# Performance work log

Measured on AMD Instinct MI355X. Metric: run time of the kernel, lower is better.

Reference implementation:

```python
import jax, jax.numpy as jnp
import numpy as np

L = 8192   # query length
N = 8192   # key/value length
DK = 128   # head dim = dmodel // h = 2048 // 16
PAD = 128  # number of trailing padded key positions


def setup_inputs() -> dict:
    key = jax.random.key(0)
    kq, kk, kv = jax.random.split(key, 3)
    Q = jax.random.normal(kq, (L, DK), dtype=jnp.float32)
    K = jax.random.normal(kk, (N, DK), dtype=jnp.float32)
    V = jax.random.normal(kv, (N, DK), dtype=jnp.float32)
    # True = masked. Causal mask (strict upper triangle) for self-attention.
    mask_self_attention = ~jnp.tril(jnp.ones((L, N), dtype=bool))
    # Padding mask: last PAD key positions are padding.
    mask_padding = jnp.zeros((L, N), dtype=bool).at[:, N - PAD:].set(True)
    return {"Q": Q, "K": K, "V": V,
            "mask_self_attention": mask_self_attention,
            "mask_padding": mask_padding}


def reference(Q, K, V, mask_self_attention, mask_padding):
    # SDPA(Q,K,V) = softmax(QK^T / sqrt(dk)) V ; dropout is identity in eval.
    scale = 1.0 / np.sqrt(DK).astype(np.float32)
    scores = (Q @ K.T) * scale                       # [L, N]
    scores = jnp.where(mask_self_attention, -jnp.inf, scores)
    scores = jnp.where(mask_padding, -jnp.inf, scores)
    attn = jax.nn.softmax(scores, axis=-1)           # [L, N]
    return attn @ V                                   # [L, DK]
```

## Files before the change

kernel.cpp:

```cpp
#include <hip/hip_runtime.h>
#include <stdint.h>

typedef __attribute__((ext_vector_type(8))) short short8;
typedef __attribute__((ext_vector_type(4))) short s16x4;
typedef __attribute__((ext_vector_type(4))) float f32x4;

#define D_K 128
#define N_KV 8192
#define NT2 64

__device__ __forceinline__ unsigned short f2bf(float x) {
  unsigned int u = __float_as_uint(x);
  u += 0x7FFFu + ((u >> 16) & 1u);
  return (unsigned short)(u >> 16);
}
__device__ __forceinline__ unsigned int pk2(float lo, float hi) {
  return (unsigned int)f2bf(lo) | ((unsigned int)f2bf(hi) << 16);
}
__device__ __forceinline__ unsigned int cvtpk(float lo, float hi) {
  unsigned int r;
  asm("v_cvt_pk_bf16_f32 %0, %1, %2" : "=v"(r) : "v"(lo), "v"(hi));
  return r;
}
__device__ __forceinline__ float bfval(unsigned int u16) {
  return __uint_as_float(u16 << 16);
}
__device__ __forceinline__ f32x4 mfma16(s16x4 a, s16x4 b, f32x4 c) {
  asm("v_mfma_f32_16x16x16_bf16 %0, %1, %2, %0" : "+v"(c) : "v"(a), "v"(b));
  return c;
}
__device__ __forceinline__ void gload16(const void* g, void* l) {
  __builtin_amdgcn_global_load_lds(
      (const __attribute__((address_space(1))) unsigned int*)g,
      (__attribute__((address_space(3))) unsigned int*)l, 16, 0, 0);
}
__device__ __host__ __forceinline__ int nunits64(int t) {
  int n = 4 * t + 4;
  return n > 252 ? 252 : n;
}

__global__ void prep_kernel(const float* __restrict__ Q,
                            const float* __restrict__ K,
                            const float* __restrict__ V,
                            unsigned short* __restrict__ Qb,
                            unsigned short* __restrict__ Kb,
                            unsigned short* __restrict__ Vtb) {
  __shared__ unsigned short tile[64][65];
  const int b = blockIdx.x;
  const int tid = threadIdx.x;
  if (b < 1024) {
    const float scale = (b < 512) ? 0.12751742941349835f : 1.0f;
    const float* src = (b < 512) ? Q : K;
    unsigned short* dst = (b < 512) ? Qb : Kb;
    const int i = (b & 511) * 256 + tid;
    const float4* s = (const float4*)src;
    float4 a = s[2 * i], c4 = s[2 * i + 1];
    uint4 o;
    o.x = pk2(a.x * scale, a.y * scale);
    o.y = pk2(a.z * scale, a.w * scale);
    o.z = pk2(c4.x * scale, c4.y * scale);
    o.w = pk2(c4.z * scale, c4.w * scale);
    *(uint4*)(dst + (size_t)i * 8) = o;
  } else {
    const int bb = b - 1024;
    const int kv0 = (bb >> 1) << 6, dk0 = (bb & 1) << 6;
    const int r = tid >> 2;
    const int c0 = (tid & 3) << 4;
#pragma unroll
    for (int j = 0; j < 4; ++j) {
      float4 v = *(const float4*)(V + (size_t)(kv0 + r) * D_K + dk0 + c0 + 4 * j);
      tile[r][c0 + 4 * j + 0] = f2bf(v.x);
      tile[r][c0 + 4 * j + 1] = f2bf(v.y);
      tile[r][c0 + 4 * j + 2] = f2bf(v.z);
      tile[r][c0 + 4 * j + 3] = f2bf(v.w);
    }
    __syncthreads();
    __align__(16) unsigned short tmp[16];
#pragma unroll
    for (int j = 0; j < 16; ++j) tmp[j] = tile[c0 + j][r];
    unsigned short* o = Vtb + (size_t)(dk0 + r) * N_KV + kv0 + c0;
    *(uint4*)(o) = *(uint4*)(tmp);
    *(uint4*)(o + 8) = *(uint4*)(tmp + 8);
  }
}

__global__ __launch_bounds__(256, 3) void attn_kernel(
    const unsigned short* __restrict__ Qb,
    const unsigned short* __restrict__ Kb,
    const unsigned short* __restrict__ Vtb,
    unsigned short* __restrict__ Opart,
    float2* __restrict__ MLpart,
    int U, int rep) {
  int rem = blockIdx.x, t = NT2 - 1;
  for (;; --t) {
    int nb = (nunits64(t) + U - 1) / U;
    if (rem < nb) break;
    rem -= nb;
  }
  const int s = rem;
  const int q0 = t << 7;
  const int n = nunits64(t);
  const int u0 = s * U;
  const int u1 = min(u0 + U, n);
  const int slot = blockIdx.x;
  const int tid = threadIdx.x;
  const int lane = tid & 63;
  const int w = tid >> 6;
  const int c = lane & 15;
  const int g = lane >> 4;
  const int qw = q0 + (w << 5);

  __shared__ __align__(16) char lds[49152];

  short8 qf[2][4];
#pragma unroll
  for (int s2 = 0; s2 < 2; ++s2) {
    const char* qrow = (const char*)(Qb + (size_t)(qw + (s2 << 4) + c) * D_K);
#pragma unroll
    for (int kc = 0; kc < 4; ++kc)
      qf[s2][kc] = *(const short8*)(qrow + kc * 64 + g * 16);
  }

  const int vo0 = ((((g >> 1) ^ ((c >> 1) & 3)) << 4) | ((g & 1) << 3));
  const int vo1 = vo0 ^ 0x20;

  int kcst[2], vcst[2], ldk[2], ldv[2];
#pragma unroll
  for (int ii = 0; ii < 2; ++ii) {
    const int ck = 2 * w + ii;
    const int rowK = (ck << 2) + (lane >> 4);
    kcst[ii] = rowK * 256 + (((lane & 15) << 4) ^ ((rowK & 7) << 4));
    ldk[ii] = ck << 10;
    const int rowV = (ck << 4) + (lane >> 2);
    const int h = (lane & 3) ^ ((lane >> 3) & 3);
    vcst[ii] = rowV * 16384 + (h << 4);
    ldv[ii] = 8192 + (ck << 10);
  }
  auto stage = [&](int u, int b) {
    char* base = lds + b * 16384;
    const int koff = (u << 5) * 256;
    const int voff = (u << 5) * 2;
#pragma unroll
    for (int ii = 0; ii < 2; ++ii) {
      gload16((const char*)Kb + koff + kcst[ii], base + ldk[ii]);
      gload16((const char*)Vtb + voff + vcst[ii], base + ldv[ii]);
    }
  };

  for (int rr = 0; rr < rep; ++rr) {
    f32x4 accT[2][8] = {};
    float m2[2] = {-3e38f, -3e38f}, lsum[2] = {0.f, 0.f};

    stage(u0, 0);
    if (u0 + 1 < u1) stage(u0 + 1, 1);
    int cb = 0;
    for (int u = u0; u < u1; ++u) {
      if (u + 1 < u1) asm volatile("s_waitcnt vmcnt(4)" ::: "memory");
      else            asm volatile("s_waitcnt vmcnt(0)" ::: "memory");
      __builtin_amdgcn_s_barrier();
      asm volatile("" ::: "memory");
      if (u + 2 < u1) {
        int nb2 = cb + 2; if (nb2 >= 3) nb2 -= 3;
        stage(u + 2, nb2);
      }
      const int kv0 = u << 5;
      char* const Kl = lds + cb * 16384;
      char* const Vl = Kl + 8192;

      if (kv0 <= qw + 31) {
        f32x4 st[2][2] = {};
        __builtin_amdgcn_s_setprio(1);
#pragma unroll
        for (int tt = 0; tt < 2; ++tt) {
          const int krow = (tt << 4) + c;
          const char* kbase = Kl + krow * 256;
          const int swk = (krow & 7) << 4;
#pragma unroll
          for (int kc = 0; kc < 4; ++kc) {
            short8 kf = *(const short8*)(kbase + ((kc * 64 + g * 16) ^ swk));
            st[0][tt] = __builtin_amdgcn_mfma_f32_16x16x32_bf16(kf, qf[0][kc], st[0][tt], 0, 0, 0);
            st[1][tt] = __builtin_amdgcn_mfma_f32_16x16x32_bf16(kf, qf[1][kc], st[1][tt], 0, 0, 0);
          }
        }
        __builtin_amdgcn_s_setprio(0);
        union PB { unsigned int u2[2]; s16x4 s4; };
        PB pb[2][2];
#pragma unroll
        for (int s2 = 0; s2 < 2; ++s2) {
          const int qws = qw + (s2 << 4);
#pragma unroll
          for (int tt = 0; tt < 2; ++tt) {
            if (kv0 + (tt << 4) + 15 > qws) {
              const int kvb = kv0 + (tt << 4) + (g << 2);
#pragma unroll
              for (int r = 0; r < 4; ++r)
                if (kvb + r > qws + c) st[s2][tt][r] = -__builtin_inff();
            }
          }
          float mx = fmaxf(fmaxf(fmaxf(st[s2][0][0], st[s2][0][1]), fmaxf(st[s2][0][2], st[s2][0][3])),
                           fmaxf(fmaxf(st[s2][1][0], st[s2][1][1]), fmaxf(st[s2][1][2], st[s2][1][3])));
          if (!__all(mx <= m2[s2] + 8.0f)) {
            float mxr = fmaxf(mx, __shfl_xor(mx, 16));
            mxr = fmaxf(mxr, __shfl_xor(mxr, 32));
            const float m2new = fmaxf(m2[s2], mxr);
            const float alpha = exp2f(m2[s2] - m2new);
            lsum[s2] *= alpha;
#pragma unroll
            for (int d = 0; d < 8; ++d)
#pragma unroll
              for (int r = 0; r < 4; ++r) accT[s2][d][r] *= alpha;
            m2[s2] = m2new;
          }
          float p[8];
#pragma unroll
          for (int tt = 0; tt < 2; ++tt)
#pragma unroll
            for (int r = 0; r < 4; ++r) {
              const float v = exp2f(st[s2][tt][r] - m2[s2]);
              p[(tt << 2) + r] = v;
              lsum[s2] += v;
            }
          pb[s2][0].u2[0] = cvtpk(p[0], p[1]);
          pb[s2][0].u2[1] = cvtpk(p[2], p[3]);
          pb[s2][1].u2[0] = cvtpk(p[4], p[5]);
          pb[s2][1].u2[1] = cvtpk(p[6], p[7]);
        }
        __builtin_amdgcn_s_setprio(1);
        {
          s16x4 va[8];
#pragma unroll
          for (int d = 0; d < 8; ++d)
            va[d] = *(const s16x4*)(Vl + (d << 10) + c * 64 + vo0);
#pragma unroll
          for (int d = 0; d < 8; ++d) accT[0][d] = mfma16(va[d], pb[0][0].s4, accT[0][d]);
#pragma unroll
          for (int d = 0; d < 8; ++d) accT[1][d] = mfma16(va[d], pb[1][0].s4, accT[1][d]);
#pragma unroll
          for (int d = 0; d < 8; ++d)
            va[d] = *(const s16x4*)(Vl + (d << 10) + c * 64 + vo1);
#pragma unroll
          for (int d = 0; d < 8; ++d) accT[0][d] = mfma16(va[d], pb[0][1].s4, accT[0][d]);
#pragma unroll
          for (int d = 0; d < 8; ++d) accT[1][d] = mfma16(va[d], pb[1][1].s4, accT[1][d]);
        }
        __builtin_amdgcn_s_setprio(0);
      }
      if (++cb == 3) cb = 0;
    }

#pragma unroll
    for (int s2 = 0; s2 < 2; ++s2) {
      float lr = lsum[s2];
      lr += __shfl_xor(lr, 16);
      lr += __shfl_xor(lr, 32);
      unsigned short* op = Opart + (size_t)slot * 16384 +
                           (size_t)((w << 5) + (s2 << 4) + c) * 128 + (g << 2);
#pragma unroll
      for (int d = 0; d < 8; ++d) {
        uint2 pk;
        pk.x = cvtpk(accT[s2][d][0], accT[s2][d][1]);
        pk.y = cvtpk(accT[s2][d][2], accT[s2][d][3]);
        *(uint2*)(op + (d << 4)) = pk;
      }
      if (lane < 16)
        MLpart[slot * 128 + (w << 5) + (s2 << 4) + lane] = make_float2(m2[s2], lr);
    }
  }
}

__global__ void combine_kernel(const unsigned short* __restrict__ Opart,
                               const float2* __restrict__ MLpart,
                               float* __restrict__ Out, int U) {
  const int gidx = blockIdx.x * 256 + threadIdx.x;
  const int q = gidx >> 5;
  const int cb = (gidx & 31) << 2;
  const int t = q >> 7, rl = q & 127;
  const int ns = (nunits64(t) + U - 1) / U;
  int base = 0;
  for (int tt = NT2 - 1; tt > t; --tt) base += (nunits64(tt) + U - 1) / U;

  float M = -3e38f;
  for (int s2 = 0; s2 < ns; ++s2)
    M = fmaxf(M, MLpart[(base + s2) * 128 + rl].x);
  float nx = 0, ny = 0, nz = 0, nw = 0, den = 0;
  for (int s2 = 0; s2 < ns; ++s2) {
    const float2 ml = MLpart[(base + s2) * 128 + rl];
    if (ml.x > -1e37f) {
      const float wg = exp2f(ml.x - M);
      den += ml.y * wg;
      const uint2 o2 = *(const uint2*)(Opart + (size_t)(base + s2) * 16384 + rl * 128 + cb);
      nx += wg * bfval(o2.x & 0xffffu);
      ny += wg * bfval(o2.x >> 16);
      nz += wg * bfval(o2.y & 0xffffu);
      nw += wg * bfval(o2.y >> 16);
    }
  }
  const float inv = 1.f / den;
  float4 r; r.x = nx * inv; r.y = ny * inv; r.z = nz * inv; r.w = nw * inv;
  *(float4*)(Out + (size_t)q * 128 + cb) = r;
}

extern "C" void kernel_launch(void* const* d_in, const int* in_sizes, int n_in,
                              void* d_out, int out_size, void* d_ws, size_t ws_size,
                              hipStream_t stream) {
  (void)in_sizes; (void)n_in; (void)out_size;
  const float* Q = (const float*)d_in[0];
  const float* K = (const float*)d_in[1];
  const float* V = (const float*)d_in[2];
  float* out = (float*)d_out;
  char* ws = (char*)d_ws;

  int U = 4;
  long slots = 0;
  for (;;) {
    slots = 0;
    for (int t = 0; t < NT2; ++t) slots += (nunits64(t) + U - 1) / U;
    size_t need = (size_t)(8u << 20) + (size_t)slots * 128 * 128 * 2;
    if ((slots <= 768 && need <= ws_size) || U >= 252) break;
    ++U;
  }

  unsigned short* Qb  = (unsigned short*)(ws);
  unsigned short* Kb  = (unsigned short*)(ws + (1u << 21));
  unsigned short* Vtb = (unsigned short*)(ws + (2u << 21));
  float2* MLp = (float2*)(ws + (3u << 21));
  unsigned short* Opb = (unsigned short*)(ws + (8u << 20));

  prep_kernel<<<1280, 256, 0, stream>>>(Q, K, V, Qb, Kb, Vtb);
  attn_kernel<<<(int)slots, 256, 0, stream>>>(Qb, Kb, Vtb, Opb, MLp, U, 1);
  combine_kernel<<<1024, 256, 0, stream>>>(Opb, MLp, out, U);
}
```

Baseline: 75.04 us.

## Drop LDS staging and read K/V tiles directly from global memory

Removes the triple-buffered global-to-LDS staging pipeline with its barriers and waitcnts. Each wave now loads its K and transposed-V fragments straight from global memory (relying on L2/L1 caching) and trims its loop bound to the causal limit per wave. This removes block-level synchronization and LDS use, which may raise occupancy. In exchange, each of the four waves fetches the same K/V data redundantly, the loads are less coalesced, and there is no prefetch to hide latency.

```diff
diff --git a/kernel.cpp b/kernel.cpp
--- a/kernel.cpp
+++ b/kernel.cpp
@@ -28,11 +28,6 @@
 __device__ __forceinline__ f32x4 mfma16(s16x4 a, s16x4 b, f32x4 c) {
   asm("v_mfma_f32_16x16x16_bf16 %0, %1, %2, %0" : "+v"(c) : "v"(a), "v"(b));
   return c;
-}
-__device__ __forceinline__ void gload16(const void* g, void* l) {
-  __builtin_amdgcn_global_load_lds(
-      (const __attribute__((address_space(1))) unsigned int*)g,
-      (__attribute__((address_space(3))) unsigned int*)l, 16, 0, 0);
 }
 __device__ __host__ __forceinline__ int nunits64(int t) {
   int n = 4 * t + 4;
@@ -90,7 +85,7 @@
     const unsigned short* __restrict__ Vtb,
     unsigned short* __restrict__ Opart,
     float2* __restrict__ MLpart,
-    int U, int rep) {
+    int U) {
   int rem = blockIdx.x, t = NT2 - 1;
   for (;; --t) {
     int nb = (nunits64(t) + U - 1) / U;
@@ -110,8 +105,6 @@
   const int g = lane >> 4;
   const int qw = q0 + (w << 5);
 
-  __shared__ __align__(16) char lds[49152];
-
   short8 qf[2][4];
 #pragma unroll
   for (int s2 = 0; s2 < 2; ++s2) {
@@ -121,150 +114,109 @@
       qf[s2][kc] = *(const short8*)(qrow + kc * 64 + g * 16);
   }
 
-  const int vo0 = ((((g >> 1) ^ ((c >> 1) & 3)) << 4) | ((g & 1) << 3));
-  const int vo1 = vo0 ^ 0x20;
-
-  int kcst[2], vcst[2], ldk[2], ldv[2];
-#pragma unroll
-  for (int ii = 0; ii < 2; ++ii) {
-    const int ck = 2 * w + ii;
-    const int rowK = (ck << 2) + (lane >> 4);
-    kcst[ii] = rowK * 256 + (((lane & 15) << 4) ^ ((rowK & 7) << 4));
-    ldk[ii] = ck << 10;
-    const int rowV = (ck << 4) + (lane >> 2);
-    const int h = (lane & 3) ^ ((lane >> 3) & 3);
-    vcst[ii] = rowV * 16384 + (h << 4);
-    ldv[ii] = 8192 + (ck << 10);
-  }
-  auto stage = [&](int u, int b) {
-    char* base = lds + b * 16384;
-    const int koff = (u << 5) * 256;
-    const int voff = (u << 5) * 2;
-#pragma unroll
-    for (int ii = 0; ii < 2; ++ii) {
-      gload16((const char*)Kb + koff + kcst[ii], base + ldk[ii]);
-      gload16((const char*)Vtb + voff + vcst[ii], base + ldv[ii]);
-    }
-  };
-
-  for (int rr = 0; rr < rep; ++rr) {
-    f32x4 accT[2][8] = {};
-    float m2[2] = {-3e38f, -3e38f}, lsum[2] = {0.f, 0.f};
-
-    stage(u0, 0);
-    if (u0 + 1 < u1) stage(u0 + 1, 1);
-    int cb = 0;
-    for (int u = u0; u < u1; ++u) {
-      if (u + 1 < u1) asm volatile("s_waitcnt vmcnt(4)" ::: "memory");
-      else            asm volatile("s_waitcnt vmcnt(0)" ::: "memory");
-      __builtin_amdgcn_s_barrier();
-      asm volatile("" ::: "memory");
-      if (u + 2 < u1) {
-        int nb2 = cb + 2; if (nb2 >= 3) nb2 -= 3;
-        stage(u + 2, nb2);
+  f32x4 accT[2][8] = {};
+  float m2[2] = {-3e38f, -3e38f}, lsum[2] = {0.f, 0.f};
+
+  const int u1w = min(u1, ((qw + 31) >> 5) + 1);
+  const char* kb = (const char*)Kb + c * 256 + g * 16;
+  const char* vb = (const char*)Vtb + (size_t)c * 16384 + (g << 3);
+
+  for (int u = u0; u < u1w; ++u) {
+    const int kv0 = u << 5;
+    f32x4 st[2][2] = {};
+    __builtin_amdgcn_s_setprio(1);
+#pragma unroll
+    for (int tt = 0; tt < 2; ++tt) {
+      const char* kr = kb + (size_t)(kv0 + (tt << 4)) * 256;
+#pragma unroll
+      for (int kc = 0; kc < 4; ++kc) {
+        const short8 kf = *(const short8*)(kr + kc * 64);
+        st[0][tt] = __builtin_amdgcn_mfma_f32_16x16x32_bf16(kf, qf[0][kc], st[0][tt], 0, 0, 0);
+        st[1][tt] = __builtin_amdgcn_mfma_f32_16x16x32_bf16(kf, qf[1][kc], st[1][tt], 0, 0, 0);
       }
-      const int kv0 = u << 5;
-      char* const Kl = lds + cb * 16384;
-      char* const Vl = Kl + 8192;
-
-      if (kv0 <= qw + 31) {
-        f32x4 st[2][2] = {};
-        __builtin_amdgcn_s_setprio(1);
-#pragma unroll
-        for (int tt = 0; tt < 2; ++tt) {
-          const int krow = (tt << 4) + c;
-          const char* kbase = Kl + krow * 256;
-          const int swk = (krow & 7) << 4;
-#pragma unroll
-          for (int kc = 0; kc < 4; ++kc) {
-            short8 kf = *(const short8*)(kbase + ((kc * 64 + g * 16) ^ swk));
-            st[0][tt] = __builtin_amdgcn_mfma_f32_16x16x32_bf16(kf, qf[0][kc], st[0][tt], 0, 0, 0);
-            st[1][tt] = __builtin_amdgcn_mfma_f32_16x16x32_bf16(kf, qf[1][kc], st[1][tt], 0, 0, 0);
-          }
+    }
+    __builtin_amdgcn_s_setprio(0);
+    union PB { unsigned int u2[2]; s16x4 s4; };
+    PB pb[2][2];
+#pragma unroll
+    for (int s2 = 0; s2 < 2; ++s2) {
+      const int qws = qw + (s2 << 4);
+#pragma unroll
+      for (int tt = 0; tt < 2; ++tt) {
+        if (kv0 + (tt << 4) + 15 > qws) {
+          const int kvb = kv0 + (tt << 4) + (g << 2);
+#pragma unroll
+          for (int r = 0; r < 4; ++r)
+            if (kvb + r > qws + c) st[s2][tt][r] = -__builtin_inff();
         }
-        __builtin_amdgcn_s_setprio(0);
-        union PB { unsigned int u2[2]; s16x4 s4; };
-        PB pb[2][2];
-#pragma unroll
-        for (int s2 = 0; s2 < 2; ++s2) {
-          const int qws = qw + (s2 << 4);
-#pragma unroll
-          for (int tt = 0; tt < 2; ++tt) {
-            if (kv0 + (tt << 4) + 15 > qws) {
-              const int kvb = kv0 + (tt << 4) + (g << 2);
-#pragma unroll
-              for (int r = 0; r < 4; ++r)
-                if (kvb + r > qws + c) st[s2][tt][r] = -__builtin_inff();
-            }
-          }
-          float mx = fmaxf(fmaxf(fmaxf(st[s2][0][0], st[s2][0][1]), fmaxf(st[s2][0][2], st[s2][0][3])),
-                           fmaxf(fmaxf(st[s2][1][0], st[s2][1][1]), fmaxf(st[s2][1][2], st[s2][1][3])));
-          if (!__all(mx <= m2[s2] + 8.0f)) {
-            float mxr = fmaxf(mx, __shfl_xor(mx, 16));
-            mxr = fmaxf(mxr, __shfl_xor(mxr, 32));
-            const float m2new = fmaxf(m2[s2], mxr);
-            const float alpha = exp2f(m2[s2] - m2new);
-            lsum[s2] *= alpha;
-#pragma unroll
-            for (int d = 0; d < 8; ++d)
-#pragma unroll
-              for (int r = 0; r < 4; ++r) accT[s2][d][r] *= alpha;
-            m2[s2] = m2new;
-          }
-          float p[8];
-#pragma unroll
-          for (int tt = 0; tt < 2; ++tt)
-#pragma unroll
-            for (int r = 0; r < 4; ++r) {
-              const float v = exp2f(st[s2][tt][r] - m2[s2]);
-              p[(tt << 2) + r] = v;
-              lsum[s2] += v;
-            }
-          pb[s2][0].u2[0] = cvtpk(p[0], p[1]);
-          pb[s2][0].u2[1] = cvtpk(p[2], p[3]);
-          pb[s2][1].u2[0] = cvtpk(p[4], p[5]);
-          pb[s2][1].u2[1] = cvtpk(p[6], p[7]);
+      }
+      float mx = fmaxf(fmaxf(fmaxf(st[s2][0][0], st[s2][0][1]), fmaxf(st[s2][0][2], st[s2][0][3])),
+                       fmaxf(fmaxf(st[s2][1][0], st[s2][1][1]), fmaxf(st[s2][1][2], st[s2][1][3])));
+      if (!__all(mx <= m2[s2] + 8.0f)) {
+        float mxr = fmaxf(mx, __shfl_xor(mx, 16));
+        mxr = fmaxf(mxr, __shfl_xor(mxr, 32));
+        const float m2new = fmaxf(m2[s2], mxr);
+        const float alpha = exp2f(m2[s2] - m2new);
+        lsum[s2] *= alpha;
+#pragma unroll
+        for (int d = 0; d < 8; ++d)
+#pragma unroll
+          for (int r = 0; r < 4; ++r) accT[s2][d][r] *= alpha;
+        m2[s2] = m2new;
+      }
+      float p[8];
+#pragma unroll
+      for (int tt = 0; tt < 2; ++tt)
+#pragma unroll
+        for (int r = 0; r < 4; ++r) {
+          const float v = exp2f(st[s2][tt][r] - m2[s2]);
+          p[(tt << 2) + r] = v;
+          lsum[s2] += v;
         }
-        __builtin_amdgcn_s_setprio(1);
-        {
-          s16x4 va[8];
-#pragma unroll
-          for (int d = 0; d < 8; ++d)
-            va[d] = *(const s16x4*)(Vl + (d << 10) + c * 64 + vo0);
-#pragma unroll
-          for (int d = 0; d < 8; ++d) accT[0][d] = mfma16(va[d], pb[0][0].s4, accT[0][d]);
-#pragma unroll
-          for (int d = 0; d < 8; ++d) accT[1][d] = mfma16(va[d], pb[1][0].s4, accT[1][d]);
-#pragma unroll
-          for (int d = 0; d < 8; ++d)
-            va[d] = *(const s16x4*)(Vl + (d << 10) + c * 64 + vo1);
-#pragma unroll
-          for (int d = 0; d < 8; ++d) accT[0][d] = mfma16(va[d], pb[0][1].s4, accT[0][d]);
-#pragma unroll
-          for (int d = 0; d < 8; ++d) accT[1][d] = mfma16(va[d], pb[1][1].s4, accT[1][d]);
-        }
-        __builtin_amdgcn_s_setprio(0);
-      }
-      if (++cb == 3) cb = 0;
-    }
-
-#pragma unroll
-    for (int s2 = 0; s2 < 2; ++s2) {
-      float lr = lsum[s2];
-      lr += __shfl_xor(lr, 16);
-      lr += __shfl_xor(lr, 32);
-      unsigned short* op = Opart + (size_t)slot * 16384 +
-                           (size_t)((w << 5) + (s2 << 4) + c) * 128 + (g << 2);
-#pragma unroll
-      for (int d = 0; d < 8; ++d) {
-        uint2 pk;
-        pk.x = cvtpk(accT[s2][d][0], accT[s2][d][1]);
-        pk.y = cvtpk(accT[s2][d][2], accT[s2][d][3]);
-        *(uint2*)(op + (d << 4)) = pk;
-      }
-      if (lane < 16)
-        MLpart[slot * 128 + (w << 5) + (s2 << 4) + lane] = make_float2(m2[s2], lr);
-    }
+      pb[s2][0].u2[0] = cvtpk(p[0], p[1]);
+      pb[s2][0].u2[1] = cvtpk(p[2], p[3]);
+      pb[s2][1].u2[0] = cvtpk(p[4], p[5]);
+      pb[s2][1].u2[1] = cvtpk(p[6], p[7]);
+    }
+    __builtin_amdgcn_s_setprio(1);
+    {
+      s16x4 va[8];
+      const char* vr0 = vb + (size_t)(kv0) * 2;
+      const char* vr1 = vb + (size_t)(kv0 + 16) * 2;
+#pragma unroll
+      for (int d = 0; d < 8; ++d)
+        va[d] = *(const s16x4*)(vr0 + ((size_t)d << 18));
+#pragma unroll
+      for (int d = 0; d < 8; ++d) accT[0][d] = mfma16(va[d], pb[0][0].s4, accT[0][d]);
+#pragma unroll
+      for (int d = 0; d < 8; ++d) accT[1][d] = mfma16(va[d], pb[1][0].s4, accT[1][d]);
+#pragma unroll
+      for (int d = 0; d < 8; ++d)
+        va[d] = *(const s16x4*)(vr1 + ((size_t)d << 18));
+#pragma unroll
+      for (int d = 0; d < 8; ++d) accT[0][d] = mfma16(va[d], pb[0][1].s4, accT[0][d]);
+#pragma unroll
+      for (int d = 0; d < 8; ++d) accT[1][d] = mfma16(va[d], pb[1][1].s4, accT[1][d]);
+    }
+    __builtin_amdgcn_s_setprio(0);
+  }
+
+#pragma unroll
+  for (int s2 = 0; s2 < 2; ++s2) {
+    float lr = lsum[s2];
+    lr += __shfl_xor(lr, 16);
+    lr += __shfl_xor(lr, 32);
+    unsigned short* op = Opart + (size_t)slot * 16384 +
+                         (size_t)((w << 5) + (s2 << 4) + c) * 128 + (g << 2);
+#pragma unroll
+    for (int d = 0; d < 8; ++d) {
+      uint2 pk;
+      pk.x = cvtpk(accT[s2][d][0], accT[s2][d][1]);
+      pk.y = cvtpk(accT[s2][d][2], accT[s2][d][3]);
+      *(uint2*)(op + (d << 4)) = pk;
+    }
+    if (lane < 16)
+      MLpart[slot * 128 + (w << 5) + (s2 << 4) + lane] = make_float2(m2[s2], lr);
   }
 }
 
@@ -327,6 +279,6 @@
   unsigned short* Opb = (unsigned short*)(ws + (8u << 20));
 
   prep_kernel<<<1280, 256, 0, stream>>>(Q, K, V, Qb, Kb, Vtb);
-  attn_kernel<<<(int)slots, 256, 0, stream>>>(Qb, Kb, Vtb, Opb, MLp, U, 1);
+  attn_kernel<<<(int)slots, 256, 0, stream>>>(Qb, Kb, Vtb, Opb, MLp, U);
   combine_kernel<<<1024, 256, 0, stream>>>(Opb, MLp, out, U);
 }
```

Result: slower. 139.0 us (+85.3%).
